# Kernel optimization log

Measured on AMD Instinct MI355X. Metric: run time of the kernel, lower is better.

Reference implementation:

```python
import jax, jax.numpy as jnp
import numpy as np

N = 100000
IN_CH = 512
HEADS = 8
OUT_CH = 1  # forced: nn.Linear(heads, 1) consumes GAT output of size heads*out_channels
E = 3200000
NEG_SLOPE = 0.2


def setup_inputs() -> dict:
    key = jax.random.key(0)
    ks = jax.random.split(key, 8)
    x = jax.random.normal(ks[0], (N, IN_CH), dtype=jnp.float32)
    edge_index = jax.random.randint(ks[1], (2, E), 0, N, dtype=jnp.int32)
    # GATConv params
    W = jax.random.normal(ks[2], (IN_CH, HEADS * OUT_CH), dtype=jnp.float32) / np.sqrt(IN_CH)
    att_src = jax.random.normal(ks[3], (HEADS, OUT_CH), dtype=jnp.float32)
    att_dst = jax.random.normal(ks[4], (HEADS, OUT_CH), dtype=jnp.float32)
    gat_bias = jnp.zeros((HEADS * OUT_CH,), dtype=jnp.float32)
    # calibration head
    lin_w = jax.random.normal(ks[5], (1, HEADS), dtype=jnp.float32) / np.sqrt(HEADS)
    lin_b = jnp.zeros((1,), dtype=jnp.float32)
    bias = jnp.ones((1,), dtype=jnp.float32)  # init bias value 1.0
    return {"x": x, "edge_index": edge_index, "W": W, "att_src": att_src,
            "att_dst": att_dst, "gat_bias": gat_bias, "lin_w": lin_w,
            "lin_b": lin_b, "bias": bias}


def reference(x, edge_index, W, att_src, att_dst, gat_bias, lin_w, lin_b, bias):
    n = x.shape[0]
    # GATConv adds self-loops by default
    loops = jnp.arange(n, dtype=edge_index.dtype)
    src = jnp.concatenate([edge_index[0], loops])
    dst = jnp.concatenate([edge_index[1], loops])

    h = (x @ W).reshape(n, HEADS, OUT_CH)                 # [N,H,C]
    a_src = (h * att_src[None]).sum(-1)                   # [N,H]
    a_dst = (h * att_dst[None]).sum(-1)                   # [N,H]

    e = jax.nn.leaky_relu(a_src[src] + a_dst[dst], NEG_SLOPE)  # [Etot,H]
    # segment softmax over incoming edges of each dst node
    e_max = jax.ops.segment_max(e, dst, num_segments=n)        # [N,H]
    e_exp = jnp.exp(e - e_max[dst])
    denom = jax.ops.segment_sum(e_exp, dst, num_segments=n)
    alpha = e_exp / (denom[dst] + 1e-16)                       # [Etot,H]

    msg = h[src] * alpha[..., None]                            # [Etot,H,C]
    out = jax.ops.segment_sum(msg, dst, num_segments=n)        # [N,H,C]
    out = out.reshape(n, HEADS * OUT_CH) + gat_bias            # concat heads

    temperature = jax.nn.relu(out @ lin_w.T + lin_b) + bias    # [N,1]
    return temperature
```

## Files before the change

kernel.cpp:

```cpp
#include <hip/hip_runtime.h>

#define IN_CH 512
#define HEADS 8
#define NEG_SLOPE 0.2f
#define STRIDE 96

__device__ __forceinline__ float lrelu(float v) {
    return v > 0.f ? v : NEG_SLOPE * v;
}

__device__ __forceinline__ void gemm_rows(const float* __restrict__ x,
                                          const float* __restrict__ W,
                                          float* __restrict__ h, int n,
                                          int wave, int nwav, int lane) {
    float4 wlo[8], whi[8];
#pragma unroll
    for (int j = 0; j < 8; ++j) {
        int k = (j < 4) ? (lane * 4 + j) : (256 + lane * 4 + (j - 4));
        const float4* p = (const float4*)(W + k * 8);
        wlo[j] = p[0];
        whi[j] = p[1];
    }
    for (int row = wave; row < n; row += nwav) {
        const float4* xr = (const float4*)(x + (size_t)row * IN_CH);
        float4 x0 = xr[lane];
        float4 x1 = xr[64 + lane];
        float xs[8] = {x0.x, x0.y, x0.z, x0.w, x1.x, x1.y, x1.z, x1.w};
        float acc[8] = {0.f, 0.f, 0.f, 0.f, 0.f, 0.f, 0.f, 0.f};
#pragma unroll
        for (int j = 0; j < 8; ++j) {
            acc[0] = fmaf(xs[j], wlo[j].x, acc[0]);
            acc[1] = fmaf(xs[j], wlo[j].y, acc[1]);
            acc[2] = fmaf(xs[j], wlo[j].z, acc[2]);
            acc[3] = fmaf(xs[j], wlo[j].w, acc[3]);
            acc[4] = fmaf(xs[j], whi[j].x, acc[4]);
            acc[5] = fmaf(xs[j], whi[j].y, acc[5]);
            acc[6] = fmaf(xs[j], whi[j].z, acc[6]);
            acc[7] = fmaf(xs[j], whi[j].w, acc[7]);
        }
#pragma unroll
        for (int off = 32; off >= 1; off >>= 1) {
#pragma unroll
            for (int hd = 0; hd < 8; ++hd)
                acc[hd] += __shfl_down(acc[hd], off, 64);
        }
        if (lane == 0) {
            float4* hp = (float4*)(h + (size_t)row * 8);
            hp[0] = make_float4(acc[0], acc[1], acc[2], acc[3]);
            hp[1] = make_float4(acc[4], acc[5], acc[6], acc[7]);
        }
    }
}

__global__ __launch_bounds__(256)
void k_fused(const float* __restrict__ x, const float* __restrict__ W,
             float* __restrict__ h, const int* __restrict__ ei,
             int* __restrict__ cnt, int* __restrict__ csr,
             int n, int E, int gemmBlocks) {
    if ((int)blockIdx.x < gemmBlocks) {
        const int lane = threadIdx.x & 63;
        const int wave = (int)((blockIdx.x * 256 + threadIdx.x) >> 6);
        gemm_rows(x, W, h, n, wave, gemmBlocks * 4, lane);
        return;
    }
    int sb = blockIdx.x - gemmBlocks;
    int base = sb * 2048 + (int)threadIdx.x * 8;
    if (base >= E) return;
    if (base + 8 <= E) {
        int4 s0 = *(const int4*)(ei + base);
        int4 s1 = *(const int4*)(ei + base + 4);
        int4 d0 = *(const int4*)(ei + E + base);
        int4 d1 = *(const int4*)(ei + E + base + 4);
        int ss[8] = {s0.x, s0.y, s0.z, s0.w, s1.x, s1.y, s1.z, s1.w};
        int dd[8] = {d0.x, d0.y, d0.z, d0.w, d1.x, d1.y, d1.z, d1.w};
        int pp[8];
#pragma unroll
        for (int k = 0; k < 8; ++k) pp[k] = atomicAdd(&cnt[dd[k]], 1);
#pragma unroll
        for (int k = 0; k < 8; ++k)
            if (pp[k] < STRIDE) csr[(size_t)dd[k] * STRIDE + pp[k]] = ss[k];
    } else {
        for (int k = 0; base + k < E; ++k) {
            int s = ei[base + k];
            int d = ei[E + base + k];
            int pos = atomicAdd(&cnt[d], 1);
            if (pos < STRIDE) csr[(size_t)d * STRIDE + pos] = s;
        }
    }
}

__global__ __launch_bounds__(256)
void k_gather(const float* __restrict__ h, const int* __restrict__ csr,
              const int* __restrict__ cnt,
              const float* __restrict__ att_src, const float* __restrict__ att_dst,
              const float* __restrict__ gat_bias, const float* __restrict__ lin_w,
              const float* __restrict__ lin_b, const float* __restrict__ bias,
              float* __restrict__ out, int n) {
    int tid = blockIdx.x * 256 + threadIdx.x;
    int node = tid >> 1;
    int sub = tid & 1;
    if (node >= n) return;

    float4 as4 = ((const float4*)att_src)[sub];
    float4 ad4 = ((const float4*)att_dst)[sub];
    float4 hi4 = ((const float4*)(h + (size_t)node * 8))[sub];
    float as[4] = {as4.x, as4.y, as4.z, as4.w};
    float ad[4] = {ad4.x, ad4.y, ad4.z, ad4.w};
    float hi[4] = {hi4.x, hi4.y, hi4.z, hi4.w};

    float hadd[4], den[4], num[4];
#pragma unroll
    for (int q = 0; q < 4; ++q) {
        hadd[q] = hi[q] * ad[q];
        float e = lrelu(hi[q] * (as[q] + ad[q]));
        float p = __expf(e);
        den[q] = p;
        num[q] = p * hi[q];
    }

    int deg = min(cnt[node], STRIDE);
    const int* row = csr + (size_t)node * STRIDE;

    int j = 0;
    for (; j + 8 <= deg; j += 8) {
        int4 c0 = *(const int4*)(row + j);
        int4 c1 = *(const int4*)(row + j + 4);
        int ss[8] = {c0.x, c0.y, c0.z, c0.w, c1.x, c1.y, c1.z, c1.w};
        float4 hs[8];
#pragma unroll
        for (int k = 0; k < 8; ++k)
            hs[k] = ((const float4*)(h + (size_t)ss[k] * 8))[sub];
#pragma unroll
        for (int k = 0; k < 8; ++k) {
            float hv[4] = {hs[k].x, hs[k].y, hs[k].z, hs[k].w};
#pragma unroll
            for (int q = 0; q < 4; ++q) {
                float e = lrelu(fmaf(hv[q], as[q], hadd[q]));
                float p = __expf(e);
                den[q] += p;
                num[q] = fmaf(p, hv[q], num[q]);
            }
        }
    }
    for (; j < deg; ++j) {
        int s = row[j];
        float4 hv4 = ((const float4*)(h + (size_t)s * 8))[sub];
        float hv[4] = {hv4.x, hv4.y, hv4.z, hv4.w};
#pragma unroll
        for (int q = 0; q < 4; ++q) {
            float e = lrelu(fmaf(hv[q], as[q], hadd[q]));
            float p = __expf(e);
            den[q] += p;
            num[q] = fmaf(p, hv[q], num[q]);
        }
    }

    float4 gb4 = ((const float4*)gat_bias)[sub];
    float4 lw4 = ((const float4*)lin_w)[sub];
    float gb[4] = {gb4.x, gb4.y, gb4.z, gb4.w};
    float lw[4] = {lw4.x, lw4.y, lw4.z, lw4.w};
    float t = 0.f;
#pragma unroll
    for (int q = 0; q < 4; ++q) {
        float o = num[q] / (den[q] + 1e-16f) + gb[q];
        t = fmaf(o, lw[q], t);
    }
    t += __shfl_xor(t, 1, 64);
    if (sub == 0) out[node] = fmaxf(t + lin_b[0], 0.f) + bias[0];
}

extern "C" void kernel_launch(void* const* d_in, const int* in_sizes, int n_in,
                              void* d_out, int out_size, void* d_ws, size_t ws_size,
                              hipStream_t stream) {
    const float* x = (const float*)d_in[0];
    const int* ei = (const int*)d_in[1];
    const float* W = (const float*)d_in[2];
    const float* att_src = (const float*)d_in[3];
    const float* att_dst = (const float*)d_in[4];
    const float* gat_bias = (const float*)d_in[5];
    const float* lin_w = (const float*)d_in[6];
    const float* lin_b = (const float*)d_in[7];
    const float* bias = (const float*)d_in[8];

    const int n = in_sizes[0] / IN_CH;
    const int E = in_sizes[1] / 2;

    float* h = (float*)d_ws;
    int* cnt = (int*)(h + (size_t)n * HEADS);
    int* csr = cnt + n;

    hipMemsetAsync(cnt, 0, (size_t)n * sizeof(int), stream);

    const int GB = 1024;
    const int SB = (E + 2047) / 2048;
    k_fused<<<GB + SB, 256, 0, stream>>>(x, W, h, ei, cnt, csr, n, E, GB);
    k_gather<<<((n * 2) + 255) / 256, 256, 0, stream>>>(
        h, csr, cnt, att_src, att_dst, gat_bias, lin_w, lin_b, bias,
        (float*)d_out, n);
}
```

Before: 440.9 us.

## Replace per-node CSR build with coarse destination buckets and shared-memory atomic aggregation

Edges are now binned into 512-node destination buckets. Each block first stages them in a shared-memory local list and then flushes them to a global bucket array with one atomic per bucket, replacing the per-node global atomics and scattered CSR writes. A new aggregation kernel assigns one 1024-thread block per bucket and accumulates softmax numerators and denominators with shared-memory float atomics. This drops the padded per-node CSR, but with only about 196 blocks it risks low occupancy and heavy LDS atomic contention, and the fixed bucket capacity could drop edges on skewed graphs.

New measurement: 668.7 us. 1.52x slower.

```diff
diff --git a/kernel.cpp b/kernel.cpp
--- a/kernel.cpp
+++ b/kernel.cpp
@@ -3,7 +3,12 @@
 #define IN_CH 512
 #define HEADS 8
 #define NEG_SLOPE 0.2f
-#define STRIDE 96
+
+#define RB 512
+#define RB_BITS 9
+#define NB_MAX 208
+#define LCAP 32
+#define BCAP 18432
 
 __device__ __forceinline__ float lrelu(float v) {
     return v > 0.f ? v : NEG_SLOPE * v;
@@ -55,118 +60,168 @@
 __global__ __launch_bounds__(256)
 void k_fused(const float* __restrict__ x, const float* __restrict__ W,
              float* __restrict__ h, const int* __restrict__ ei,
-             int* __restrict__ cnt, int* __restrict__ csr,
-             int n, int E, int gemmBlocks) {
+             int* __restrict__ gtail, int* __restrict__ bucket,
+             int n, int E, int gemmBlocks, int nb) {
     if ((int)blockIdx.x < gemmBlocks) {
         const int lane = threadIdx.x & 63;
         const int wave = (int)((blockIdx.x * 256 + threadIdx.x) >> 6);
         gemm_rows(x, W, h, n, wave, gemmBlocks * 4, lane);
         return;
     }
+
+    __shared__ int lcnt[NB_MAX];
+    __shared__ int gbase[NB_MAX];
+    __shared__ int lst[NB_MAX * LCAP];
+
+    for (int i = threadIdx.x; i < nb; i += 256) lcnt[i] = 0;
+    __syncthreads();
+
     int sb = blockIdx.x - gemmBlocks;
     int base = sb * 2048 + (int)threadIdx.x * 8;
-    if (base >= E) return;
-    if (base + 8 <= E) {
-        int4 s0 = *(const int4*)(ei + base);
-        int4 s1 = *(const int4*)(ei + base + 4);
-        int4 d0 = *(const int4*)(ei + E + base);
-        int4 d1 = *(const int4*)(ei + E + base + 4);
-        int ss[8] = {s0.x, s0.y, s0.z, s0.w, s1.x, s1.y, s1.z, s1.w};
-        int dd[8] = {d0.x, d0.y, d0.z, d0.w, d1.x, d1.y, d1.z, d1.w};
-        int pp[8];
-#pragma unroll
-        for (int k = 0; k < 8; ++k) pp[k] = atomicAdd(&cnt[dd[k]], 1);
-#pragma unroll
-        for (int k = 0; k < 8; ++k)
-            if (pp[k] < STRIDE) csr[(size_t)dd[k] * STRIDE + pp[k]] = ss[k];
-    } else {
-        for (int k = 0; base + k < E; ++k) {
-            int s = ei[base + k];
-            int d = ei[E + base + k];
-            int pos = atomicAdd(&cnt[d], 1);
-            if (pos < STRIDE) csr[(size_t)d * STRIDE + pos] = s;
-        }
-    }
-}
-
-__global__ __launch_bounds__(256)
-void k_gather(const float* __restrict__ h, const int* __restrict__ csr,
-              const int* __restrict__ cnt,
-              const float* __restrict__ att_src, const float* __restrict__ att_dst,
-              const float* __restrict__ gat_bias, const float* __restrict__ lin_w,
-              const float* __restrict__ lin_b, const float* __restrict__ bias,
-              float* __restrict__ out, int n) {
-    int tid = blockIdx.x * 256 + threadIdx.x;
-    int node = tid >> 1;
-    int sub = tid & 1;
-    if (node >= n) return;
-
-    float4 as4 = ((const float4*)att_src)[sub];
-    float4 ad4 = ((const float4*)att_dst)[sub];
-    float4 hi4 = ((const float4*)(h + (size_t)node * 8))[sub];
-    float as[4] = {as4.x, as4.y, as4.z, as4.w};
-    float ad[4] = {ad4.x, ad4.y, ad4.z, ad4.w};
-    float hi[4] = {hi4.x, hi4.y, hi4.z, hi4.w};
-
-    float hadd[4], den[4], num[4];
-#pragma unroll
-    for (int q = 0; q < 4; ++q) {
-        hadd[q] = hi[q] * ad[q];
-        float e = lrelu(hi[q] * (as[q] + ad[q]));
-        float p = __expf(e);
-        den[q] = p;
-        num[q] = p * hi[q];
-    }
-
-    int deg = min(cnt[node], STRIDE);
-    const int* row = csr + (size_t)node * STRIDE;
-
-    int j = 0;
-    for (; j + 8 <= deg; j += 8) {
-        int4 c0 = *(const int4*)(row + j);
-        int4 c1 = *(const int4*)(row + j + 4);
-        int ss[8] = {c0.x, c0.y, c0.z, c0.w, c1.x, c1.y, c1.z, c1.w};
-        float4 hs[8];
-#pragma unroll
-        for (int k = 0; k < 8; ++k)
-            hs[k] = ((const float4*)(h + (size_t)ss[k] * 8))[sub];
-#pragma unroll
-        for (int k = 0; k < 8; ++k) {
-            float hv[4] = {hs[k].x, hs[k].y, hs[k].z, hs[k].w};
-#pragma unroll
-            for (int q = 0; q < 4; ++q) {
-                float e = lrelu(fmaf(hv[q], as[q], hadd[q]));
-                float p = __expf(e);
-                den[q] += p;
-                num[q] = fmaf(p, hv[q], num[q]);
+    if (base < E) {
+        if (base + 8 <= E) {
+            int4 s0 = *(const int4*)(ei + base);
+            int4 s1 = *(const int4*)(ei + base + 4);
+            int4 d0 = *(const int4*)(ei + E + base);
+            int4 d1 = *(const int4*)(ei + E + base + 4);
+            int ss[8] = {s0.x, s0.y, s0.z, s0.w, s1.x, s1.y, s1.z, s1.w};
+            int dd[8] = {d0.x, d0.y, d0.z, d0.w, d1.x, d1.y, d1.z, d1.w};
+#pragma unroll
+            for (int k = 0; k < 8; ++k) {
+                int d = dd[k];
+                int b = d >> RB_BITS;
+                int v = (ss[k] << RB_BITS) | (d & (RB - 1));
+                int p = atomicAdd(&lcnt[b], 1);
+                if (p < LCAP) {
+                    lst[b * LCAP + p] = v;
+                } else {
+                    int g = atomicAdd(&gtail[b], 1);
+                    if (g < BCAP) bucket[(size_t)b * BCAP + g] = v;
+                }
             }
-        }
-    }
-    for (; j < deg; ++j) {
-        int s = row[j];
-        float4 hv4 = ((const float4*)(h + (size_t)s * 8))[sub];
-        float hv[4] = {hv4.x, hv4.y, hv4.z, hv4.w};
-#pragma unroll
-        for (int q = 0; q < 4; ++q) {
-            float e = lrelu(fmaf(hv[q], as[q], hadd[q]));
-            float p = __expf(e);
-            den[q] += p;
-            num[q] = fmaf(p, hv[q], num[q]);
-        }
-    }
-
-    float4 gb4 = ((const float4*)gat_bias)[sub];
-    float4 lw4 = ((const float4*)lin_w)[sub];
-    float gb[4] = {gb4.x, gb4.y, gb4.z, gb4.w};
-    float lw[4] = {lw4.x, lw4.y, lw4.z, lw4.w};
-    float t = 0.f;
-#pragma unroll
-    for (int q = 0; q < 4; ++q) {
-        float o = num[q] / (den[q] + 1e-16f) + gb[q];
-        t = fmaf(o, lw[q], t);
-    }
-    t += __shfl_xor(t, 1, 64);
-    if (sub == 0) out[node] = fmaxf(t + lin_b[0], 0.f) + bias[0];
+        } else {
+            for (int k = 0; k < 8 && base + k < E; ++k) {
+                int s = ei[base + k];
+                int d = ei[E + base + k];
+                int b = d >> RB_BITS;
+                int v = (s << RB_BITS) | (d & (RB - 1));
+                int p = atomicAdd(&lcnt[b], 1);
+                if (p < LCAP) {
+                    lst[b * LCAP + p] = v;
+                } else {
+                    int g = atomicAdd(&gtail[b], 1);
+                    if (g < BCAP) bucket[(size_t)b * BCAP + g] = v;
+                }
+            }
+        }
+    }
+    __syncthreads();
+
+    for (int b = threadIdx.x; b < nb; b += 256) {
+        int c = min(lcnt[b], LCAP);
+        gbase[b] = c ? atomicAdd(&gtail[b], c) : 0;
+    }
+    __syncthreads();
+
+    int tot = nb * LCAP;
+    for (int pr = threadIdx.x; pr < tot; pr += 256) {
+        int b = pr >> 5;
+        int i = pr & (LCAP - 1);
+        if (i < min(lcnt[b], LCAP)) {
+            int pos = gbase[b] + i;
+            if (pos < BCAP) bucket[(size_t)b * BCAP + pos] = lst[b * LCAP + i];
+        }
+    }
+}
+
+__global__ __launch_bounds__(1024)
+void k_agg(const float* __restrict__ h, const int* __restrict__ bucket,
+           const int* __restrict__ gtail,
+           const float* __restrict__ att_src, const float* __restrict__ att_dst,
+           const float* __restrict__ gat_bias, const float* __restrict__ lin_w,
+           const float* __restrict__ lin_b, const float* __restrict__ bias,
+           float* __restrict__ out, int n) {
+    __shared__ float acc[16][RB];
+    __shared__ float hw[8][RB];
+
+    const int b = blockIdx.x;
+    const int base = b << RB_BITS;
+    const int Wn = min(RB, n - base);
+
+    for (int i = threadIdx.x; i < 16 * RB; i += 1024)
+        (&acc[0][0])[i] = 0.f;
+    for (int i = threadIdx.x; i < Wn * 8; i += 1024)
+        hw[i & 7][i >> 3] = h[(size_t)(base + (i >> 3)) * 8 + (i & 7)];
+    __syncthreads();
+
+    float as[8], ad[8];
+#pragma unroll
+    for (int q = 0; q < 8; ++q) { as[q] = att_src[q]; ad[q] = att_dst[q]; }
+
+    const int tail = min(gtail[b], BCAP);
+    const int* __restrict__ lstp = bucket + (size_t)b * BCAP;
+
+    int i = threadIdx.x;
+    for (; i + 1024 < tail; i += 2048) {
+        int v0 = lstp[i], v1 = lstp[i + 1024];
+        int s0 = v0 >> RB_BITS, d0 = v0 & (RB - 1);
+        int s1 = v1 >> RB_BITS, d1 = v1 & (RB - 1);
+        const float4* p0 = (const float4*)(h + (size_t)s0 * 8);
+        const float4* p1 = (const float4*)(h + (size_t)s1 * 8);
+        float4 a0 = p0[0], b0 = p0[1];
+        float4 a1 = p1[0], b1 = p1[1];
+        float hs0[8] = {a0.x, a0.y, a0.z, a0.w, b0.x, b0.y, b0.z, b0.w};
+        float hs1[8] = {a1.x, a1.y, a1.z, a1.w, b1.x, b1.y, b1.z, b1.w};
+#pragma unroll
+        for (int q = 0; q < 8; ++q) {
+            float e = lrelu(fmaf(hs0[q], as[q], hw[q][d0] * ad[q]));
+            float p = __expf(e);
+            atomicAdd(&acc[q][d0], p * hs0[q]);
+            atomicAdd(&acc[8 + q][d0], p);
+        }
+#pragma unroll
+        for (int q = 0; q < 8; ++q) {
+            float e = lrelu(fmaf(hs1[q], as[q], hw[q][d1] * ad[q]));
+            float p = __expf(e);
+            atomicAdd(&acc[q][d1], p * hs1[q]);
+            atomicAdd(&acc[8 + q][d1], p);
+        }
+    }
+    for (; i < tail; i += 1024) {
+        int v = lstp[i];
+        int s = v >> RB_BITS, dl = v & (RB - 1);
+        const float4* hp = (const float4*)(h + (size_t)s * 8);
+        float4 ha = hp[0], hb = hp[1];
+        float hs[8] = {ha.x, ha.y, ha.z, ha.w, hb.x, hb.y, hb.z, hb.w};
+#pragma unroll
+        for (int q = 0; q < 8; ++q) {
+            float e = lrelu(fmaf(hs[q], as[q], hw[q][dl] * ad[q]));
+            float p = __expf(e);
+            atomicAdd(&acc[q][dl], p * hs[q]);
+            atomicAdd(&acc[8 + q][dl], p);
+        }
+    }
+    __syncthreads();
+
+    float gb[8], lw[8];
+#pragma unroll
+    for (int q = 0; q < 8; ++q) { gb[q] = gat_bias[q]; lw[q] = lin_w[q]; }
+    float lb = lin_b[0], bs = bias[0];
+
+    for (int ln = threadIdx.x; ln < Wn; ln += 1024) {
+        float t = 0.f;
+#pragma unroll
+        for (int q = 0; q < 8; ++q) {
+            float hv = hw[q][ln];
+            float e = lrelu(hv * (as[q] + ad[q]));
+            float p = __expf(e);
+            float num = fmaf(p, hv, acc[q][ln]);
+            float den = acc[8 + q][ln] + p;
+            float o = num / (den + 1e-16f) + gb[q];
+            t = fmaf(o, lw[q], t);
+        }
+        out[base + ln] = fmaxf(t + lb, 0.f) + bs;
+    }
 }
 
 extern "C" void kernel_launch(void* const* d_in, const int* in_sizes, int n_in,
@@ -184,17 +239,18 @@
 
     const int n = in_sizes[0] / IN_CH;
     const int E = in_sizes[1] / 2;
+    const int nb = (n + RB - 1) >> RB_BITS;
 
     float* h = (float*)d_ws;
-    int* cnt = (int*)(h + (size_t)n * HEADS);
-    int* csr = cnt + n;
-
-    hipMemsetAsync(cnt, 0, (size_t)n * sizeof(int), stream);
+    int* gtail = (int*)(h + (size_t)n * HEADS);
+    int* bucket = gtail + 256;
+
+    hipMemsetAsync(gtail, 0, nb * sizeof(int), stream);
 
     const int GB = 1024;
     const int SB = (E + 2047) / 2048;
-    k_fused<<<GB + SB, 256, 0, stream>>>(x, W, h, ei, cnt, csr, n, E, GB);
-    k_gather<<<((n * 2) + 255) / 256, 256, 0, stream>>>(
-        h, csr, cnt, att_src, att_dst, gat_bias, lin_w, lin_b, bias,
-        (float*)d_out, n);
-}
+    k_fused<<<GB + SB, 256, 0, stream>>>(x, W, h, ei, gtail, bucket, n, E, GB, nb);
+    k_agg<<<nb, 1024, 0, stream>>>(h, bucket, gtail, att_src, att_dst,
+                                   gat_bias, lin_w, lin_b, bias,
+                                   (float*)d_out, n);
+}
```
